# Optimization experiments

Measured on AMD Instinct MI355X. Metric: run time of the kernel, lower is better.

The kernel has to match this reference:

```python
import jax, jax.numpy as jnp
import numpy as np

D_MODEL = 2048
N_HEADS = 16
D_K = D_MODEL // N_HEADS  # 128


def setup_inputs() -> dict:
    key = jax.random.key(0)
    ks = jax.random.split(key, 12)
    B, S = 2, 2048
    std = 1.0 / np.sqrt(D_MODEL)
    inp = {
        "query": jax.random.normal(ks[0], (B, S, D_MODEL), jnp.float32),
        "key": jax.random.normal(ks[1], (B, S, D_MODEL), jnp.float32),
        "value": jax.random.normal(ks[2], (B, S, D_MODEL), jnp.float32),
        "w_q": jax.random.normal(ks[3], (D_MODEL, D_MODEL), jnp.float32) * std,
        "b_q": jnp.zeros((D_MODEL,), jnp.float32),
        "w_k": jax.random.normal(ks[4], (D_MODEL, D_MODEL), jnp.float32) * std,
        "b_k": jnp.zeros((D_MODEL,), jnp.float32),
        "w_v": jax.random.normal(ks[5], (D_MODEL, D_MODEL), jnp.float32) * std,
        "b_v": jnp.zeros((D_MODEL,), jnp.float32),
        "w_o": jax.random.normal(ks[6], (D_MODEL, D_MODEL), jnp.float32) * std,
        "b_o": jnp.zeros((D_MODEL,), jnp.float32),
        # fractional scale numerator / denominator per head; ratio ~ 1/sqrt(d_k)
        "scale_alpha": jnp.full((N_HEADS,), 1.0, jnp.float32),
        "scale_beta": jnp.full((N_HEADS,), float(np.sqrt(D_K)), jnp.float32),
    }
    return inp


def reference(query, key, value, w_q, b_q, w_k, b_k, w_v, b_v, w_o, b_o,
              scale_alpha, scale_beta):
    B, S, _ = query.shape
    # projections (torch Linear: x @ W^T + b)
    Q = (query @ w_q.T + b_q).reshape(B, S, N_HEADS, D_K).transpose(0, 2, 1, 3)
    K = (key @ w_k.T + b_k).reshape(B, S, N_HEADS, D_K).transpose(0, 2, 1, 3)
    V = (value @ w_v.T + b_v).reshape(B, S, N_HEADS, D_K).transpose(0, 2, 1, 3)
    # per-head fractional scale alpha/beta (computed under no_grad in torch)
    scales = jax.lax.stop_gradient(scale_alpha / jnp.maximum(scale_beta, 1.0))
    scores = jnp.einsum("bhqd,bhkd->bhqk", Q, K) * scales[None, :, None, None]
    attn = jax.nn.softmax(scores, axis=-1)  # dropout is identity in eval
    out = jnp.einsum("bhqk,bhkd->bhqd", attn, V)
    out = out.transpose(0, 2, 1, 3).reshape(B, S, D_MODEL)
    return out @ w_o.T + b_o
```

## Files before the change

### kernel.cpp

```cpp
#include <hip/hip_runtime.h>
#include <cstdint>

#define S_LEN   2048
#define DMODEL  2048
#define NHEADS  16
#define DK      128
#define MROWS   4096

typedef _Float16 f16;
using f16x8 = __attribute__((ext_vector_type(8))) _Float16;
using f16x4 = __attribute__((ext_vector_type(4))) _Float16;
using f32x4 = __attribute__((ext_vector_type(4))) float;

typedef const __attribute__((address_space(1))) unsigned int gu32;
typedef __attribute__((address_space(3))) unsigned int lu32;

__device__ __forceinline__ void gl2lds16(const void* g, void* l) {
    __builtin_amdgcn_global_load_lds((gu32*)g, (lu32*)l, 16, 0, 0);
}

__global__ __launch_bounds__(256) void cvt_all(
    const float* __restrict__ q, const float* __restrict__ k,
    const float* __restrict__ v, const float* __restrict__ wq,
    const float* __restrict__ wk, const float* __restrict__ wv,
    const float* __restrict__ wo,
    f16* cq, f16* ck, f16* cv, f16* cwq, f16* cwk, f16* cwv, f16* cwo)
{
    const int b = blockIdx.x;
    const float* src; f16* dst; int base;
    if      (b <  8192) { src = q;  dst = cq;  base = b; }
    else if (b < 16384) { src = k;  dst = ck;  base = b - 8192; }
    else if (b < 24576) { src = v;  dst = cv;  base = b - 16384; }
    else if (b < 28672) { src = wq; dst = cwq; base = b - 24576; }
    else if (b < 32768) { src = wk; dst = cwk; base = b - 28672; }
    else if (b < 36864) { src = wv; dst = cwv; base = b - 32768; }
    else                { src = wo; dst = cwo; base = b - 36864; }
    const int i = base * 256 + threadIdx.x;
    float4 x = ((const float4*)src)[i];
    f16x4 o; o[0] = (f16)x.x; o[1] = (f16)x.y; o[2] = (f16)x.z; o[3] = (f16)x.w;
    ((f16x4*)dst)[i] = o;
}

#define NT_K (DMODEL / 32)

template<int BN>
__device__ __forceinline__ void gemm_core2(
    const f16* __restrict__ A, const f16* __restrict__ W,
    const float* __restrict__ bias, void* __restrict__ Cout,
    int mode, const float* __restrict__ sa, const float* __restrict__ sb)
{
    constexpr int NJ = BN / 64;
    __shared__ f16 As[4][256 * 32];
    __shared__ f16 Bs[4][BN * 32];

    const int tid  = threadIdx.x;
    const int wid  = tid >> 6;
    const int ln   = tid & 15;
    const int quad = (tid & 63) >> 4;
    const int wm   = (wid >> 2) * 128;
    const int wn   = (wid & 3) * (16 * NJ);
    const int bm   = blockIdx.y * 256;
    const int bn   = blockIdx.x * BN;
    const int K = DMODEL, N = DMODEL;

    f32x4 acc[8][NJ];
#pragma unroll
    for (int i = 0; i < 8; ++i)
#pragma unroll
        for (int j = 0; j < NJ; ++j)
            acc[i][j] = (f32x4){0.f, 0.f, 0.f, 0.f};

    const int sr  = tid >> 2;
    const int kcs = ((tid & 3) ^ ((tid >> 3) & 3)) * 8;
    const f16* gA0 = A + (size_t)(bm + sr) * K + kcs;
    const f16* gA1 = A + (size_t)(bm + 128 + sr) * K + kcs;
    const f16* gB0 = W + (size_t)(bn + sr) * K + kcs;
    const f16* gB1 = W + (size_t)(bn + 128 + sr) * K + kcs;
    const int koff = (quad ^ ((ln >> 1) & 3)) * 8;

#define STAGE_A(t_) do { const int b_ = (t_) & 3; const int k_ = (t_) * 32; \
        gl2lds16(gA0 + k_, &As[b_][tid * 8]);                               \
        gl2lds16(gA1 + k_, &As[b_][4096 + tid * 8]); } while (0)
#define STAGE_B(t_) do { const int b_ = (t_) & 3; const int k_ = (t_) * 32; \
        gl2lds16(gB0 + k_, &Bs[b_][tid * 8]);                               \
        if (BN == 256) gl2lds16(gB1 + k_, &Bs[b_][4096 + tid * 8]); } while (0)

    STAGE_A(0); STAGE_B(0);
    STAGE_A(1); STAGE_B(1);
    STAGE_A(2); STAGE_B(2);

    for (int t = 0; t < NT_K; ++t) {
        const f16* Ab = As[t & 3];
        const f16* Bb = Bs[t & 3];
        if (BN == 256) {
            if (t < NT_K - 2)       asm volatile("s_waitcnt vmcnt(8)" ::: "memory");
            else if (t == NT_K - 2) asm volatile("s_waitcnt vmcnt(4)" ::: "memory");
            else                    asm volatile("s_waitcnt vmcnt(0)" ::: "memory");
        } else {
            if (t < NT_K - 2)       asm volatile("s_waitcnt vmcnt(6)" ::: "memory");
            else if (t == NT_K - 2) asm volatile("s_waitcnt vmcnt(3)" ::: "memory");
            else                    asm volatile("s_waitcnt vmcnt(0)" ::: "memory");
        }
        __builtin_amdgcn_s_barrier();
        __builtin_amdgcn_sched_barrier(0);

        f16x8 af[4], bf[NJ];
#pragma unroll
        for (int i = 0; i < 4; ++i)
            af[i] = *(const f16x8*)&Ab[(wm + i * 16 + ln) * 32 + koff];
#pragma unroll
        for (int j = 0; j < NJ; ++j)
            bf[j] = *(const f16x8*)&Bb[(wn + j * 16 + ln) * 32 + koff];
        if (t + 3 < NT_K) STAGE_A(t + 3);
        asm volatile("s_waitcnt lgkmcnt(0)" ::: "memory");
        __builtin_amdgcn_sched_barrier(0);
        __builtin_amdgcn_s_setprio(1);
#pragma unroll
        for (int i = 0; i < 4; ++i)
#pragma unroll
            for (int j = 0; j < NJ; ++j)
                acc[i][j] = __builtin_amdgcn_mfma_f32_16x16x32_f16(
                    af[i], bf[j], acc[i][j], 0, 0, 0);
        __builtin_amdgcn_s_setprio(0);

#pragma unroll
        for (int i = 0; i < 4; ++i)
            af[i] = *(const f16x8*)&Ab[(wm + (4 + i) * 16 + ln) * 32 + koff];
        if (t + 3 < NT_K) STAGE_B(t + 3);
        asm volatile("s_waitcnt lgkmcnt(0)" ::: "memory");
        __builtin_amdgcn_sched_barrier(0);
        __builtin_amdgcn_s_setprio(1);
#pragma unroll
        for (int i = 0; i < 4; ++i)
#pragma unroll
            for (int j = 0; j < NJ; ++j)
                acc[4 + i][j] = __builtin_amdgcn_mfma_f32_16x16x32_f16(
                    af[i], bf[j], acc[4 + i][j], 0, 0, 0);
        __builtin_amdgcn_s_setprio(0);
    }
#undef STAGE_A
#undef STAGE_B

#pragma unroll
    for (int j = 0; j < NJ; ++j) {
        const int n = bn + wn + j * 16 + ln;
        const float bn_ = bias[n];
        const int h = n >> 7;
        const int d = n & (DK - 1);
        float scq = 1.0f;
        if (mode == 3) scq = sa[h] / fmaxf(sb[h], 1.0f);
#pragma unroll
        for (int i = 0; i < 8; ++i) {
#pragma unroll
            for (int reg = 0; reg < 4; ++reg) {
                const int m = bm + wm + i * 16 + quad * 4 + reg;
                float v = acc[i][j][reg] + bn_;
                if (mode == 0) {
                    ((float*)Cout)[(size_t)m * N + n] = v;
                } else {
                    const int bb = m >> 11;
                    const int ss = m & (S_LEN - 1);
                    size_t idx;
                    if (mode == 2)
                        idx = (((size_t)(bb * NHEADS + h) * DK + d) * S_LEN + ss);
                    else
                        idx = (((size_t)(bb * NHEADS + h) * S_LEN + ss) * DK + d);
                    if (mode == 3) v *= scq;
                    ((f16*)Cout)[idx] = (f16)v;
                }
            }
        }
    }
}

__global__ __launch_bounds__(512, 2) void qkv_gemm(
    const f16* Aq, const f16* Ak, const f16* Av,
    const f16* Wq, const f16* Wk, const f16* Wv,
    const float* bq, const float* bk, const float* bv,
    f16* Oq, f16* Ok, f16* Ov, const float* sa, const float* sb)
{
    const int z = blockIdx.z;
    const f16* A = (z == 0) ? Aq : (z == 1) ? Ak : Av;
    const f16* W = (z == 0) ? Wq : (z == 1) ? Wk : Wv;
    const float* bias = (z == 0) ? bq : (z == 1) ? bk : bv;
    void* O = (z == 0) ? (void*)Oq : (z == 1) ? (void*)Ok : (void*)Ov;
    const int mode = (z == 0) ? 3 : (z == 1) ? 1 : 2;
    gemm_core2<256>(A, W, bias, O, mode, sa, sb);
}

__global__ __launch_bounds__(512, 2) void out_gemm(
    const f16* A, const f16* W, const float* bias, float* O)
{
    gemm_core2<128>(A, W, bias, O, 0, nullptr, nullptr);
}

__global__ __launch_bounds__(256, 2) void flash_v4(
    const f16* __restrict__ Qg, const f16* __restrict__ Kg,
    const f16* __restrict__ VTg, f16* __restrict__ AO)
{
    __shared__ f16 Ks[4 * 64 * 32];
    __shared__ f16 Vs[2 * 128 * 32];
    __shared__ f16 Ps[2 * 128 * 32];
    __shared__ float l_buf[2 * 128];

    const int tid = threadIdx.x;
    const int wid = tid >> 6;
    const int ln = tid & 15;
    const int quad = (tid & 63) >> 4;
    const int wq = wid & 1;
    const int wc = wid >> 1;
    const int bh = blockIdx.y;
    const int q0 = blockIdx.x * 128;

    const int koff = (quad ^ ((ln >> 1) & 3)) * 8;
    const int soff_sw = ((tid & 3) ^ ((tid >> 3) & 3)) * 8;

    f16x8 qf[4][4];
    const f16* Qbase = Qg + ((size_t)bh * S_LEN + q0 + wq * 64) * DK;
#pragma unroll
    for (int nt = 0; nt < 4; ++nt)
#pragma unroll
        for (int kc = 0; kc < 4; ++kc)
            qf[nt][kc] = *(const f16x8*)(Qbase + (size_t)(nt * 16 + ln) * DK
                                         + kc * 32 + quad * 8);

    f32x4 o[4][4];
    float lp[4] = {0.f, 0.f, 0.f, 0.f};
#pragma unroll
    for (int i = 0; i < 4; ++i)
#pragma unroll
        for (int j = 0; j < 4; ++j)
            o[i][j] = (f32x4){0.f, 0.f, 0.f, 0.f};

    const f16* Kgb = Kg + (size_t)bh * S_LEN * DK;
    const f16* Vgb = VTg + (size_t)bh * DK * S_LEN;
    const int srow = tid >> 2;

    for (int kt = 0; kt < S_LEN / 64; ++kt) {
        __syncthreads();
#pragma unroll
        for (int j = 0; j < 4; ++j)
            gl2lds16(Kgb + (size_t)(kt * 64 + srow) * DK + j * 32 + soff_sw,
                     Ks + j * 2048 + tid * 8);
#pragma unroll
        for (int j = 0; j < 4; ++j)
            gl2lds16(Vgb + (size_t)(srow + (j & 1) * 64) * S_LEN
                         + kt * 64 + (j >> 1) * 32 + soff_sw,
                     Vs + (j >> 1) * 4096 + (j & 1) * 2048 + tid * 8);
        __syncthreads();

        f32x4 s[2][4];
#pragma unroll
        for (int mt = 0; mt < 2; ++mt)
#pragma unroll
            for (int nt = 0; nt < 4; ++nt)
                s[mt][nt] = (f32x4){0.f, 0.f, 0.f, 0.f};
        __builtin_amdgcn_s_setprio(1);
#pragma unroll
        for (int kc = 0; kc < 4; ++kc) {
            f16x8 kf0 = *(const f16x8*)&Ks[kc * 2048 + (wc * 32 + ln) * 32 + koff];
            f16x8 kf1 = *(const f16x8*)&Ks[kc * 2048 + (wc * 32 + 16 + ln) * 32 + koff];
#pragma unroll
            for (int nt = 0; nt < 4; ++nt) {
                s[0][nt] = __builtin_amdgcn_mfma_f32_16x16x32_f16(kf0, qf[nt][kc], s[0][nt], 0, 0, 0);
                s[1][nt] = __builtin_amdgcn_mfma_f32_16x16x32_f16(kf1, qf[nt][kc], s[1][nt], 0, 0, 0);
            }
        }
        __builtin_amdgcn_s_setprio(0);

#pragma unroll
        for (int mt = 0; mt < 2; ++mt) {
#pragma unroll
            for (int nt = 0; nt < 4; ++nt) {
                const float p0 = __expf(s[mt][nt][0]);
                const float p1 = __expf(s[mt][nt][1]);
                const float p2 = __expf(s[mt][nt][2]);
                const float p3 = __expf(s[mt][nt][3]);
                lp[nt] += (p0 + p1) + (p2 + p3);
                f16x4 pk;
                pk[0] = (f16)p0; pk[1] = (f16)p1; pk[2] = (f16)p2; pk[3] = (f16)p3;
                const int pchunk = ((mt * 2 + (quad >> 1)) ^ ((ln >> 1) & 3)) * 8
                                   + (quad & 1) * 4;
                *(f16x4*)&Ps[wc * 4096 + (wq * 64 + nt * 16 + ln) * 32 + pchunk] = pk;
            }
        }
        __syncthreads();

        __builtin_amdgcn_s_setprio(1);
#pragma unroll
        for (int cc = 0; cc < 2; ++cc) {
            f16x8 pf[4];
#pragma unroll
            for (int mtq = 0; mtq < 4; ++mtq)
                pf[mtq] = *(const f16x8*)&Ps[cc * 4096 + (wq * 64 + mtq * 16 + ln) * 32 + koff];
#pragma unroll
            for (int ntd = 0; ntd < 4; ++ntd) {
                f16x8 vf = *(const f16x8*)&Vs[cc * 4096 + (wc * 64 + ntd * 16 + ln) * 32 + koff];
#pragma unroll
                for (int mtq = 0; mtq < 4; ++mtq)
                    o[mtq][ntd] = __builtin_amdgcn_mfma_f32_16x16x32_f16(
                        pf[mtq], vf, o[mtq][ntd], 0, 0, 0);
            }
        }
        __builtin_amdgcn_s_setprio(0);
    }

#pragma unroll
    for (int nt = 0; nt < 4; ++nt) {
        float v = lp[nt];
        v += __shfl_xor(v, 16, 64);
        v += __shfl_xor(v, 32, 64);
        lp[nt] = v;
    }
    if (quad == 0) {
#pragma unroll
        for (int nt = 0; nt < 4; ++nt)
            l_buf[wc * 128 + wq * 64 + nt * 16 + ln] = lp[nt];
    }
    __syncthreads();

    const int b = bh >> 4;
    const int h = bh & (NHEADS - 1);
#pragma unroll
    for (int mtq = 0; mtq < 4; ++mtq) {
#pragma unroll
        for (int reg = 0; reg < 4; ++reg) {
            const int ql = wq * 64 + mtq * 16 + quad * 4 + reg;
            const float inv = 1.0f / (l_buf[ql] + l_buf[128 + ql]);
            f16* dst = AO + ((size_t)b * S_LEN + q0 + ql) * DMODEL + h * DK + wc * 64;
#pragma unroll
            for (int ntd = 0; ntd < 4; ++ntd)
                dst[ntd * 16 + ln] = (f16)(o[mtq][ntd][reg] * inv);
        }
    }
}

extern "C" void kernel_launch(void* const* d_in, const int* in_sizes, int n_in,
                              void* d_out, int out_size, void* d_ws, size_t ws_size,
                              hipStream_t stream)
{
    (void)in_sizes; (void)n_in; (void)out_size; (void)ws_size;
    const float* query = (const float*)d_in[0];
    const float* key_  = (const float*)d_in[1];
    const float* value = (const float*)d_in[2];
    const float* w_q = (const float*)d_in[3];
    const float* b_q = (const float*)d_in[4];
    const float* w_k = (const float*)d_in[5];
    const float* b_k = (const float*)d_in[6];
    const float* w_v = (const float*)d_in[7];
    const float* b_v = (const float*)d_in[8];
    const float* w_o = (const float*)d_in[9];
    const float* b_o = (const float*)d_in[10];
    const float* s_alpha = (const float*)d_in[11];
    const float* s_beta  = (const float*)d_in[12];
    float* out = (float*)d_out;

    const size_t T = (size_t)MROWS * DMODEL;
    const size_t Wn = (size_t)DMODEL * DMODEL;
    f16* base = (f16*)d_ws;
    f16* c_q = base;
    f16* c_k = base + T;
    f16* c_v = base + 2 * T;
    f16* Qh  = base + 3 * T;
    f16* wq16 = base + 4 * T;
    f16* wk16 = wq16 + Wn;
    f16* wv16 = wk16 + Wn;
    f16* wo16 = wv16 + Wn;
    f16* Kh  = (f16*)d_out;
    f16* VT  = Kh + T;
    f16* AOh = c_v;

    cvt_all<<<dim3(40960), dim3(256), 0, stream>>>(
        query, key_, value, w_q, w_k, w_v, w_o,
        c_q, c_k, c_v, wq16, wk16, wv16, wo16);

    dim3 qkv_grid(DMODEL / 256, MROWS / 256, 3);
    qkv_gemm<<<qkv_grid, dim3(512), 0, stream>>>(c_q, c_k, c_v, wq16, wk16, wv16,
                                                 b_q, b_k, b_v, Qh, Kh, VT,
                                                 s_alpha, s_beta);

    dim3 flash_grid(S_LEN / 128, 2 * NHEADS);
    flash_v4<<<flash_grid, dim3(256), 0, stream>>>(Qh, Kh, VT, AOh);

    dim3 out_grid(DMODEL / 128, MROWS / 256);
    out_gemm<<<out_grid, dim3(512), 0, stream>>>(AOh, wo16, b_o, out);
}
```

Before: 484.3 us.

## Restructure projection GEMMs to double-buffered 64-wide K tiles with XCD-aware block swizzle

Rewrites the GEMM core so each main-loop iteration covers a 64-wide K slice split into two 32-wide halves, double-buffered instead of the previous four-stage 32-wide ring. For the BN=128 case the B tile uses a 64-wide row layout with an 8-way XOR swizzle. Block indices are remapped so consecutive blocks, which land on different XCDs, share A/B tiles and get better L2 reuse. The cost is more barriers per iteration and a shallower prefetch distance, which may expose memory latency.

After: 517.9 us. 1.07x slower.

```diff
diff --git a/kernel.cpp b/kernel.cpp
--- a/kernel.cpp
+++ b/kernel.cpp
@@ -6,6 +6,7 @@
 #define NHEADS  16
 #define DK      128
 #define MROWS   4096
+#define NKT     (DMODEL / 64)
 
 typedef _Float16 f16;
 using f16x8 = __attribute__((ext_vector_type(8))) _Float16;
@@ -41,17 +42,16 @@
     ((f16x4*)dst)[i] = o;
 }
 
-#define NT_K (DMODEL / 32)
-
 template<int BN>
-__device__ __forceinline__ void gemm_core2(
+__device__ __forceinline__ void gemm8(
     const f16* __restrict__ A, const f16* __restrict__ W,
     const float* __restrict__ bias, void* __restrict__ Cout,
-    int mode, const float* __restrict__ sa, const float* __restrict__ sb)
+    int mode, const float* __restrict__ sa, const float* __restrict__ sb,
+    int bx, int by)
 {
     constexpr int NJ = BN / 64;
-    __shared__ f16 As[4][256 * 32];
-    __shared__ f16 Bs[4][BN * 32];
+    __shared__ f16 As[4 * 8192];
+    __shared__ f16 Bs[(BN == 256 ? 4 : 2) * 8192];
 
     const int tid  = threadIdx.x;
     const int wid  = tid >> 6;
@@ -59,9 +59,9 @@
     const int quad = (tid & 63) >> 4;
     const int wm   = (wid >> 2) * 128;
     const int wn   = (wid & 3) * (16 * NJ);
-    const int bm   = blockIdx.y * 256;
-    const int bn   = blockIdx.x * BN;
-    const int K = DMODEL, N = DMODEL;
+    const int bm   = by * 256;
+    const int bn   = bx * BN;
+    const int K    = DMODEL;
 
     f32x4 acc[8][NJ];
 #pragma unroll
@@ -70,83 +70,124 @@
         for (int j = 0; j < NJ; ++j)
             acc[i][j] = (f32x4){0.f, 0.f, 0.f, 0.f};
 
-    const int sr  = tid >> 2;
-    const int kcs = ((tid & 3) ^ ((tid >> 3) & 3)) * 8;
-    const f16* gA0 = A + (size_t)(bm + sr) * K + kcs;
-    const f16* gA1 = A + (size_t)(bm + 128 + sr) * K + kcs;
-    const f16* gB0 = W + (size_t)(bn + sr) * K + kcs;
-    const f16* gB1 = W + (size_t)(bn + 128 + sr) * K + kcs;
     const int koff = (quad ^ ((ln >> 1) & 3)) * 8;
-
-#define STAGE_A(t_) do { const int b_ = (t_) & 3; const int k_ = (t_) * 32; \
-        gl2lds16(gA0 + k_, &As[b_][tid * 8]);                               \
-        gl2lds16(gA1 + k_, &As[b_][4096 + tid * 8]); } while (0)
-#define STAGE_B(t_) do { const int b_ = (t_) & 3; const int k_ = (t_) * 32; \
-        gl2lds16(gB0 + k_, &Bs[b_][tid * 8]);                               \
-        if (BN == 256) gl2lds16(gB1 + k_, &Bs[b_][4096 + tid * 8]); } while (0)
-
-    STAGE_A(0); STAGE_B(0);
-    STAGE_A(1); STAGE_B(1);
-    STAGE_A(2); STAGE_B(2);
-
-    for (int t = 0; t < NT_K; ++t) {
-        const f16* Ab = As[t & 3];
-        const f16* Bb = Bs[t & 3];
-        if (BN == 256) {
-            if (t < NT_K - 2)       asm volatile("s_waitcnt vmcnt(8)" ::: "memory");
-            else if (t == NT_K - 2) asm volatile("s_waitcnt vmcnt(4)" ::: "memory");
-            else                    asm volatile("s_waitcnt vmcnt(0)" ::: "memory");
-        } else {
-            if (t < NT_K - 2)       asm volatile("s_waitcnt vmcnt(6)" ::: "memory");
-            else if (t == NT_K - 2) asm volatile("s_waitcnt vmcnt(3)" ::: "memory");
-            else                    asm volatile("s_waitcnt vmcnt(0)" ::: "memory");
-        }
-        __builtin_amdgcn_s_barrier();
-        __builtin_amdgcn_sched_barrier(0);
-
+    const int kcs4 = ((tid & 3) ^ ((tid >> 3) & 3)) * 8;
+    const int kcs8 = ((tid & 7) ^ ((tid >> 3) & 7)) * 8;
+    const f16* gA = A + (size_t)(bm + (tid >> 2)) * K + kcs4;
+    const f16* gB = (BN == 256)
+        ? W + (size_t)(bn + (tid >> 2)) * K + kcs4
+        : W + (size_t)(bn + (tid >> 3)) * K + kcs8;
+
+#define SA_(t_, kh_) do { \
+    f16* dst_ = &As[(((t_) & 1) * 2 + (kh_)) * 8192]; \
+    const f16* g_ = gA + (t_) * 64 + (kh_) * 32; \
+    gl2lds16(g_,                   dst_ + tid * 8); \
+    gl2lds16(g_ + (size_t)128 * K, dst_ + (tid + 512) * 8); } while (0)
+
+#define SB256_(t_, kh_) do { \
+    f16* dst_ = &Bs[(((t_) & 1) * 2 + (kh_)) * 8192]; \
+    const f16* g_ = gB + (t_) * 64 + (kh_) * 32; \
+    gl2lds16(g_,                   dst_ + tid * 8); \
+    gl2lds16(g_ + (size_t)128 * K, dst_ + (tid + 512) * 8); } while (0)
+
+#define SB128_(t_) do { \
+    f16* dst_ = &Bs[((t_) & 1) * 8192]; \
+    const f16* g_ = gB + (t_) * 64; \
+    gl2lds16(g_,                  dst_ + tid * 8); \
+    gl2lds16(g_ + (size_t)64 * K, dst_ + (tid + 512) * 8); } while (0)
+
+#define LDA_(d_, kh_, R_) do { \
+    const f16* p_ = &As[((d_) * 2 + (kh_)) * 8192]; \
+    _Pragma("unroll") \
+    for (int i_ = 0; i_ < 4; ++i_) \
+        af[i_] = *(const f16x8*)&p_[(wm + ((R_) + i_) * 16 + ln) * 32 + koff]; \
+    } while (0)
+
+#define LDB_(d_, kh_) do { \
+    if constexpr (BN == 256) { \
+        const f16* p_ = &Bs[((d_) * 2 + (kh_)) * 8192]; \
+        _Pragma("unroll") \
+        for (int j_ = 0; j_ < NJ; ++j_) \
+            bf[j_] = *(const f16x8*)&p_[(wn + j_ * 16 + ln) * 32 + koff]; \
+    } else { \
+        const f16* p_ = &Bs[(d_) * 8192]; \
+        _Pragma("unroll") \
+        for (int j_ = 0; j_ < NJ; ++j_) \
+            bf[j_] = *(const f16x8*)&p_[(wn + j_ * 16 + ln) * 64 \
+                         + ((((kh_) * 4 + quad) ^ (ln & 7)) * 8)]; \
+    } } while (0)
+
+#define MF_(R_) do { \
+    __builtin_amdgcn_s_setprio(1); \
+    _Pragma("unroll") \
+    for (int i_ = 0; i_ < 4; ++i_) \
+    _Pragma("unroll") \
+        for (int j_ = 0; j_ < NJ; ++j_) \
+            acc[(R_) + i_][j_] = __builtin_amdgcn_mfma_f32_16x16x32_f16( \
+                af[i_], bf[j_], acc[(R_) + i_][j_], 0, 0, 0); \
+    __builtin_amdgcn_s_setprio(0); } while (0)
+
+#define BAR_  __builtin_amdgcn_s_barrier()
+#define SBAR_ __builtin_amdgcn_sched_barrier(0)
+#define LGKM0_ do { asm volatile("s_waitcnt lgkmcnt(0)" ::: "memory"); SBAR_; } while (0)
+
+    SA_(0, 0);
+    if constexpr (BN == 256) SB256_(0, 0); else SB128_(0);
+    SA_(0, 1);
+    if constexpr (BN == 256) SB256_(0, 1);
+    if constexpr (BN == 256) asm volatile("s_waitcnt vmcnt(4)" ::: "memory");
+    else                     asm volatile("s_waitcnt vmcnt(2)" ::: "memory");
+    BAR_; SBAR_;
+
+    for (int t = 0; t < NKT; ++t) {
+        const int d = t & 1;
+        const bool nl = (t + 1 < NKT);
         f16x8 af[4], bf[NJ];
-#pragma unroll
-        for (int i = 0; i < 4; ++i)
-            af[i] = *(const f16x8*)&Ab[(wm + i * 16 + ln) * 32 + koff];
-#pragma unroll
-        for (int j = 0; j < NJ; ++j)
-            bf[j] = *(const f16x8*)&Bb[(wn + j * 16 + ln) * 32 + koff];
-        if (t + 3 < NT_K) STAGE_A(t + 3);
-        asm volatile("s_waitcnt lgkmcnt(0)" ::: "memory");
-        __builtin_amdgcn_sched_barrier(0);
-        __builtin_amdgcn_s_setprio(1);
-#pragma unroll
-        for (int i = 0; i < 4; ++i)
-#pragma unroll
-            for (int j = 0; j < NJ; ++j)
-                acc[i][j] = __builtin_amdgcn_mfma_f32_16x16x32_f16(
-                    af[i], bf[j], acc[i][j], 0, 0, 0);
-        __builtin_amdgcn_s_setprio(0);
-
-#pragma unroll
-        for (int i = 0; i < 4; ++i)
-            af[i] = *(const f16x8*)&Ab[(wm + (4 + i) * 16 + ln) * 32 + koff];
-        if (t + 3 < NT_K) STAGE_B(t + 3);
-        asm volatile("s_waitcnt lgkmcnt(0)" ::: "memory");
-        __builtin_amdgcn_sched_barrier(0);
-        __builtin_amdgcn_s_setprio(1);
-#pragma unroll
-        for (int i = 0; i < 4; ++i)
-#pragma unroll
-            for (int j = 0; j < NJ; ++j)
-                acc[4 + i][j] = __builtin_amdgcn_mfma_f32_16x16x32_f16(
-                    af[i], bf[j], acc[4 + i][j], 0, 0, 0);
-        __builtin_amdgcn_s_setprio(0);
-    }
-#undef STAGE_A
-#undef STAGE_B
-
+
+        LDB_(d, 0); LDA_(d, 0, 0);
+        if (nl) SA_(t + 1, 0);
+        BAR_; LGKM0_; MF_(0);
+        BAR_;
+
+        LDA_(d, 0, 4);
+        if (nl) { if constexpr (BN == 256) SB256_(t + 1, 0); else SB128_(t + 1); }
+        BAR_; LGKM0_; MF_(4);
+        if (nl) asm volatile("s_waitcnt vmcnt(4)" ::: "memory");
+        else    asm volatile("s_waitcnt vmcnt(0)" ::: "memory");
+        BAR_; SBAR_;
+
+        LDB_(d, 1); LDA_(d, 1, 0);
+        if (nl) SA_(t + 1, 1);
+        BAR_; LGKM0_; MF_(0);
+        BAR_;
+
+        LDA_(d, 1, 4);
+        if (nl) { if constexpr (BN == 256) SB256_(t + 1, 1); }
+        BAR_; LGKM0_; MF_(4);
+        if (nl) {
+            if constexpr (BN == 256) asm volatile("s_waitcnt vmcnt(4)" ::: "memory");
+            else                     asm volatile("s_waitcnt vmcnt(2)" ::: "memory");
+        }
+        BAR_; SBAR_;
+    }
+
+#undef SA_
+#undef SB256_
+#undef SB128_
+#undef LDA_
+#undef LDB_
+#undef MF_
+#undef BAR_
+#undef SBAR_
+#undef LGKM0_
+
+    const int N = DMODEL;
 #pragma unroll
     for (int j = 0; j < NJ; ++j) {
         const int n = bn + wn + j * 16 + ln;
         const float bn_ = bias[n];
         const int h = n >> 7;
-        const int d = n & (DK - 1);
+        const int dd = n & (DK - 1);
         float scq = 1.0f;
         if (mode == 3) scq = sa[h] / fmaxf(sb[h], 1.0f);
 #pragma unroll
@@ -162,9 +203,9 @@
                     const int ss = m & (S_LEN - 1);
                     size_t idx;
                     if (mode == 2)
-                        idx = (((size_t)(bb * NHEADS + h) * DK + d) * S_LEN + ss);
+                        idx = (((size_t)(bb * NHEADS + h) * DK + dd) * S_LEN + ss);
                     else
-                        idx = (((size_t)(bb * NHEADS + h) * S_LEN + ss) * DK + d);
+                        idx = (((size_t)(bb * NHEADS + h) * S_LEN + ss) * DK + dd);
                     if (mode == 3) v *= scq;
                     ((f16*)Cout)[idx] = (f16)v;
                 }
@@ -179,19 +220,25 @@
     const float* bq, const float* bk, const float* bv,
     f16* Oq, f16* Ok, f16* Ov, const float* sa, const float* sb)
 {
-    const int z = blockIdx.z;
+    const int lin = blockIdx.x + (blockIdx.y << 3) + (blockIdx.z << 7);
+    const int swz = (lin & 7) * 48 + (lin >> 3);
+    const int bx = swz & 7, by = (swz >> 3) & 15, z = swz >> 7;
+
     const f16* A = (z == 0) ? Aq : (z == 1) ? Ak : Av;
     const f16* W = (z == 0) ? Wq : (z == 1) ? Wk : Wv;
     const float* bias = (z == 0) ? bq : (z == 1) ? bk : bv;
     void* O = (z == 0) ? (void*)Oq : (z == 1) ? (void*)Ok : (void*)Ov;
     const int mode = (z == 0) ? 3 : (z == 1) ? 1 : 2;
-    gemm_core2<256>(A, W, bias, O, mode, sa, sb);
+    gemm8<256>(A, W, bias, O, mode, sa, sb, bx, by);
 }
 
 __global__ __launch_bounds__(512, 2) void out_gemm(
     const f16* A, const f16* W, const float* bias, float* O)
 {
-    gemm_core2<128>(A, W, bias, O, 0, nullptr, nullptr);
+    const int lin = blockIdx.x + (blockIdx.y << 4);
+    const int swz = (lin & 7) * 32 + (lin >> 3);
+    const int bx = swz & 15, by = swz >> 4;
+    gemm8<128>(A, W, bias, O, 0, nullptr, nullptr, bx, by);
 }
 
 __global__ __launch_bounds__(256, 2) void flash_v4(
```
